# Kernel tuning notes

Hardware: AMD Instinct MI355X
Metric: run time of the kernel (lower is better)

The kernel has to match this reference:

```python
import jax, jax.numpy as jnp
import numpy as np
from jax import lax

# ---- config (mirrors cfg.* used by the module) ----
ANCHOR_RATIOS = (0.5, 1.0, 2.0)
ANCHOR_SCALES = (8.0, 16.0, 32.0)
FEATURE_STRIDE = 16
BASE_SIZE = 40  # generate_anchors(40, ...)
BN_EPS = 1e-5
LOG_CLAMP = 1e-30  # torch uses 1e-300, which underflows to 0 in fp32; use fp32-safe tiny


def generate_anchors(base_size=BASE_SIZE, ratios=ANCHOR_RATIOS, scales=ANCHOR_SCALES):
    """py-faster-rcnn style anchor generation, corner format (x1,y1,x2,y2). -> (A,4)"""
    w = h = float(base_size)
    cx = (base_size - 1) * 0.5
    cy = (base_size - 1) * 0.5
    size = w * h
    out = []
    for r in ratios:
        ws = np.round(np.sqrt(size / r))
        hs = np.round(ws * r)
        for s in scales:
            W, H = ws * s, hs * s
            out.append([cx - 0.5 * (W - 1), cy - 0.5 * (H - 1),
                        cx + 0.5 * (W - 1), cy + 0.5 * (H - 1)])
    return np.asarray(out, dtype=np.float32)  # (A,4)


def splash_anchors(fH, fW, n, base_anchors, stride):
    """Shift base anchors over the feature grid. -> (n, fH*fW*A, 4), row-major H,W then A."""
    sx = jnp.arange(fW, dtype=jnp.float32) * stride
    sy = jnp.arange(fH, dtype=jnp.float32) * stride
    SY, SX = jnp.meshgrid(sy, sx, indexing='ij')            # (fH,fW)
    shifts = jnp.stack([SX, SY, SX, SY], axis=-1).reshape(-1, 1, 4)  # (fH*fW,1,4)
    anc = (shifts + jnp.asarray(base_anchors)[None, :, :]).reshape(-1, 4)  # (fH*fW*A,4)
    return jnp.broadcast_to(anc[None], (n, anc.shape[0], 4))


def conv2d(x, w, b, pad):
    y = lax.conv_general_dilated(x, w, (1, 1), [(pad, pad), (pad, pad)],
                                 dimension_numbers=('NCHW', 'OIHW', 'NCHW'))
    return y + b[None, :, None, None]


def batchnorm_train(x, gamma, beta):
    # training-mode BN: per-channel batch stats over (N,H,W), biased variance
    m = jnp.mean(x, axis=(0, 2, 3), keepdims=True)
    v = jnp.mean(jnp.square(x - m), axis=(0, 2, 3), keepdims=True)
    xn = (x - m) * lax.rsqrt(v + BN_EPS)
    return xn * gamma[None, :, None, None] + beta[None, :, None, None]


def mish(x):
    return x * jnp.tanh(jax.nn.softplus(x))


def corner2center(b):
    w = b[..., 2] - b[..., 0]
    h = b[..., 3] - b[..., 1]
    cx = b[..., 0] + 0.5 * w
    cy = b[..., 1] + 0.5 * h
    return jnp.stack([cx, cy, w, h], axis=-1)


def setup_inputs() -> dict:
    key = jax.random.key(0)
    ks = jax.random.split(key, 7)
    C_IN, C_BASE, A = 256, 256, 9
    x = jax.random.normal(ks[0], (8, C_IN, 128, 128), dtype=jnp.float32)
    # kaiming-uniform-ish scaled weights
    def kaiming(k, shape):
        fan_in = shape[1] * shape[2] * shape[3]
        bound = float(np.sqrt(6.0 / fan_in))
        return jax.random.uniform(k, shape, jnp.float32, -bound, bound)
    return {
        "x": x,
        "W_base": kaiming(ks[1], (C_BASE, C_IN, 3, 3)),
        "b_base": jnp.zeros((C_BASE,), jnp.float32),
        "g_base": jnp.ones((C_BASE,), jnp.float32),
        "be_base": jnp.zeros((C_BASE,), jnp.float32),
        "W_cls": kaiming(ks[2], (2 * A, C_BASE, 1, 1)),
        "b_cls": jnp.zeros((2 * A,), jnp.float32),
        "g_cls": jnp.ones((2 * A,), jnp.float32),
        "be_cls": jnp.zeros((2 * A,), jnp.float32),
        "W_reg": kaiming(ks[3], (4 * A, C_BASE, 1, 1)),
        "b_reg": jnp.zeros((4 * A,), jnp.float32),
        "g_reg": jnp.ones((4 * A,), jnp.float32),
        "be_reg": jnp.zeros((4 * A,), jnp.float32),
        "img_size": 2048,
    }


def reference(x, W_base, b_base, g_base, be_base,
              W_cls, b_cls, g_cls, be_cls,
              W_reg, b_reg, g_reg, be_reg, img_size):
    n, c, fH, fW = x.shape
    A = 9
    # BASE_CONV: Conv3x3 -> Mish -> Dropout2d (identity here, deterministic) -> BN
    base = batchnorm_train(mish(conv2d(x, W_base, b_base, 1)), g_base, be_base)

    anchors = splash_anchors(fH, fW, n, generate_anchors(), FEATURE_STRIDE)  # (n,K,4) corners

    rpn_reg = batchnorm_train(conv2d(base, W_reg, b_reg, 0), g_reg, be_reg)
    rpn_reg = jnp.transpose(rpn_reg, (0, 2, 3, 1)).reshape(n, -1, 4)          # (n,K,4)

    rpn_score = batchnorm_train(conv2d(base, W_cls, b_cls, 0), g_cls, be_cls)
    rpn_score = jnp.transpose(rpn_score, (0, 2, 3, 1)).reshape(n, fH, fW, A, 2)
    fg_scores = jax.nn.softmax(rpn_score, axis=4)[..., 1].reshape(n, -1)      # (n,K)

    rpn_reg = rpn_reg + anchors                                               # decoded corners

    # proposal layer: clip proposals to the image, keep all (fixed-shape)
    lim = jnp.float32(img_size)
    rois = jnp.clip(rpn_reg, 0.0, lim)                                        # (n,K,4) corners
    rois = corner2center(rois)                                                # (cx,cy,w,h)

    anc_c = corner2center(anchors)
    tx = (rois[..., 0] - anc_c[..., 0]) / anc_c[..., 2]
    ty = (rois[..., 1] - anc_c[..., 1]) / anc_c[..., 3]
    tw = jnp.log(jnp.maximum(rois[..., 2] / anc_c[..., 2], LOG_CLAMP))
    th = jnp.log(jnp.maximum(rois[..., 3] / anc_c[..., 3], LOG_CLAMP))
    ts = jnp.stack([tx, ty, tw, th], axis=-1)
    return (fg_scores, ts, rois)
```

## Files before the change

### kernel.cpp

```cpp
#include <hip/hip_runtime.h>
#include <stdint.h>

typedef short bf16x8 __attribute__((ext_vector_type(8)));
typedef float f32x4 __attribute__((ext_vector_type(4)));

#define AS1 __attribute__((address_space(1)))
#define AS3 __attribute__((address_space(3)))

static __device__ __forceinline__ void gl16(const void* g, void* l) {
  __builtin_amdgcn_global_load_lds((const AS1 void*)g, (AS3 void*)l, 16, 0, 0);
}

static __device__ __forceinline__ unsigned short f2bf(float f) {
  unsigned u = __float_as_uint(f);
  u = u + 0x7fffu + ((u >> 16) & 1u);
  return (unsigned short)(u >> 16);
}
static __device__ __forceinline__ float bf2f(unsigned short h) {
  return __uint_as_float(((unsigned)h) << 16);
}
static __device__ __forceinline__ float mishf(float x) {
  float sp = fmaxf(x, 0.f) + log1pf(expf(-fabsf(x)));
  float e2 = expf(-2.f * sp);
  float th = (1.f - e2) / (1.f + e2);
  return x * th;
}

#define NIMG 8
#define HH 128
#define WW 128
#define HP 130
#define CIN 256
#define MPIX (NIMG * HH * WW)
#define KTOT 2304
#define FGCNT (MPIX * 9)
#define TSCNT (MPIX * 9 * 4)

__device__ __constant__ float AW[9] = {456.f, 912.f, 1824.f, 320.f, 640.f, 1280.f, 224.f, 448.f, 896.f};
__device__ __constant__ float AH[9] = {224.f, 448.f, 896.f, 320.f, 640.f, 1280.f, 448.f, 896.f, 1792.f};

__global__ __launch_bounds__(256) void k_wt(const float* __restrict__ Wb,
                                            unsigned short* __restrict__ Wt2) {
  int d = blockIdx.x * 256 + threadIdx.x;
  int c = d & 31, oc = (d >> 5) & 255, s = d >> 13;
  int kh = s / 24, r = s % 24, kw = r >> 3, icb = r & 7;
  int ic = icb * 32 + c;
  Wt2[d] = f2bf(Wb[((oc * 256 + ic) * 3 + kh) * 3 + kw]);
}

__global__ __launch_bounds__(256) void k_tr(const float* __restrict__ x,
                                            unsigned short* __restrict__ xt2) {
  __shared__ float tile[32][129];
  int b = blockIdx.x;
  int icb = b & 7, h = (b >> 3) & 127, n = b >> 10;
  int t = threadIdx.x;
  const float* src = x + (((size_t)(n * 256 + icb * 32) * 128 + h) * 128);
#pragma unroll
  for (int i = 0; i < 4; ++i) {
    int idx = t + 256 * i;
    int w4 = idx & 31, ic = idx >> 5;
    float4 v = *(const float4*)(src + (size_t)ic * 16384 + w4 * 4);
    tile[ic][w4 * 4 + 0] = v.x; tile[ic][w4 * 4 + 1] = v.y;
    tile[ic][w4 * 4 + 2] = v.z; tile[ic][w4 * 4 + 3] = v.w;
  }
  __syncthreads();
#pragma unroll
  for (int i = 0; i < 8; ++i) {
    int idx = t + 256 * i;
    int icp = idx & 15, w = idx >> 4;
    unsigned lo = f2bf(tile[icp * 2][w]);
    unsigned hi = f2bf(tile[icp * 2 + 1][w]);
    size_t pix = ((size_t)(icb * 8 + n) * HP + (h + 1)) * HP + (w + 1);
    *(unsigned*)(xt2 + pix * 32 + icp * 2) = lo | (hi << 16);
  }
}

__global__ __launch_bounds__(256) void k_bord(unsigned short* __restrict__ xt2) {
  int tid = blockIdx.x * 256 + threadIdx.x;
  int chunk = tid & 3, pix = tid >> 2;
  int nn = pix / 516, bp = pix % 516;
  int hp, wp;
  if (bp < 130) { hp = 0; wp = bp; }
  else if (bp < 260) { hp = 129; wp = bp - 130; }
  else { int r = bp - 260; hp = 1 + (r >> 1); wp = (r & 1) ? 129 : 0; }
  size_t off = (((size_t)nn * HP + hp) * HP + wp) * 32 + chunk * 8;
  uint4 z = {0u, 0u, 0u, 0u};
  *(uint4*)(xt2 + off) = z;
}

__global__ __launch_bounds__(512) void k_conv(const unsigned short* __restrict__ xt2,
                                              const unsigned short* __restrict__ Wt2,
                                              const float* __restrict__ b_base,
                                              unsigned short* __restrict__ yt2,
                                              float* __restrict__ statsA) {
  __shared__ __align__(16) char lds[49152];
  char* aldsb = lds;
  char* bldsb = lds + 16384;
  int t = threadIdx.x;
  int lane = t & 63, w4 = t >> 6;
  int wr = w4 >> 2, wc = w4 & 3;
  int row16 = lane & 15, kgl = lane >> 4;
  int mq = (row16 & 3) ^ ((row16 >> 2) & 3);
  int kq16 = (kgl ^ mq) * 16;

  int bid = blockIdx.x;
  int swz = (bid & 7) * 128 + (bid >> 3);
  int n = swz >> 7, h0 = swz & 127;
  size_t M0 = (size_t)swz * 128;

  f32x4 acc[4][4];
#pragma unroll
  for (int m = 0; m < 4; ++m)
#pragma unroll
    for (int nf = 0; nf < 4; ++nf) { f32x4 z = {0.f, 0.f, 0.f, 0.f}; acc[m][nf] = z; }

  int pixA = t >> 2;
  int qA = (t & 3) ^ ((pixA & 3) ^ ((pixA >> 2) & 3));
  char* dA = aldsb + w4 * 1024;
  char* dB0 = bldsb + w4 * 1024;
  char* dB1 = bldsb + 8192 + w4 * 1024;

  auto STAGE = [&](int sv, int c_) {
    int kh_ = sv / 24, r_ = sv % 24, kw_ = r_ >> 3, icb_ = r_ & 7;
    const unsigned short* pa = xt2 +
        (((size_t)(icb_ * 8 + n) * HP + h0 + kh_) * HP + pixA + kw_) * 32 + qA * 8;
    gl16(pa, dA + c_ * 8192);
    const unsigned short* pb = Wt2 + ((size_t)sv * 256 + pixA) * 32 + qA * 8;
    gl16(pb, dB0 + c_ * 16384);
    gl16(pb + 4096, dB1 + c_ * 16384);
  };

  STAGE(0, 0);
  asm volatile("s_waitcnt vmcnt(0)" ::: "memory");
  __builtin_amdgcn_s_barrier();
  __builtin_amdgcn_sched_barrier(0);

  int cur = 0;
  for (int s2 = 0; s2 < 72; ++s2) {
    if (s2 < 71) STAGE(s2 + 1, cur ^ 1);
    const char* ab = aldsb + cur * 8192;
    const char* bb2 = bldsb + cur * 16384;
    bf16x8 af[4], bfr[4];
#pragma unroll
    for (int m = 0; m < 4; ++m)
      af[m] = *(const bf16x8*)(ab + (wr * 64 + m * 16 + row16) * 64 + kq16);
#pragma unroll
    for (int nf = 0; nf < 4; ++nf)
      bfr[nf] = *(const bf16x8*)(bb2 + (wc * 64 + nf * 16 + row16) * 64 + kq16);
    asm volatile("s_waitcnt lgkmcnt(0)" ::: "memory");
    __builtin_amdgcn_sched_barrier(0);
    __builtin_amdgcn_s_setprio(1);
#pragma unroll
    for (int m = 0; m < 4; ++m)
#pragma unroll
      for (int nf = 0; nf < 4; ++nf)
        acc[m][nf] = __builtin_amdgcn_mfma_f32_16x16x32_bf16(af[m], bfr[nf], acc[m][nf], 0, 0, 0);
    __builtin_amdgcn_s_setprio(0);
    if (s2 < 71) {
      asm volatile("s_waitcnt vmcnt(0)" ::: "memory");
      __builtin_amdgcn_s_barrier();
      __builtin_amdgcn_sched_barrier(0);
    }
    cur ^= 1;
  }

  float sums[4] = {0.f, 0.f, 0.f, 0.f}, sumq[4] = {0.f, 0.f, 0.f, 0.f};
#pragma unroll
  for (int nf = 0; nf < 4; ++nf) {
    int oc = wc * 64 + nf * 16 + row16;
    float bias = b_base[oc];
    size_t obase = (size_t)(oc >> 5) * MPIX * 32 + (oc & 31);
#pragma unroll
    for (int m = 0; m < 4; ++m) {
#pragma unroll
      for (int j = 0; j < 4; ++j) {
        int p = wr * 64 + m * 16 + kgl * 4 + j;
        float y = mishf(acc[m][nf][j] + bias);
        yt2[obase + (M0 + p) * 32] = f2bf(y);
        sums[nf] += y; sumq[nf] += y * y;
      }
    }
  }
#pragma unroll
  for (int nf = 0; nf < 4; ++nf) {
    float s1 = sums[nf], s2 = sumq[nf];
    s1 += __shfl_xor(s1, 16); s2 += __shfl_xor(s2, 16);
    s1 += __shfl_xor(s1, 32); s2 += __shfl_xor(s2, 32);
    if (lane < 16) {
      int oc = wc * 64 + nf * 16 + lane;
      atomicAdd(&statsA[oc], s1);
      atomicAdd(&statsA[256 + oc], s2);
    }
  }
}

__global__ __launch_bounds__(256) void k_fold(const float* __restrict__ statsA,
                                              const float* __restrict__ g_base,
                                              const float* __restrict__ be_base,
                                              const float* __restrict__ W_cls,
                                              const float* __restrict__ b_cls,
                                              const float* __restrict__ W_reg,
                                              const float* __restrict__ b_reg,
                                              unsigned short* __restrict__ W2t2,
                                              float* __restrict__ b2) {
  __shared__ float sS[256], sT[256];
  int t = threadIdx.x;
  {
    float cnt = (float)MPIX;
    float m = statsA[t] / cnt;
    float v = fmaxf(statsA[256 + t] / cnt - m * m, 0.f);
    float s = g_base[t] * rsqrtf(v + 1e-5f);
    sS[t] = s;
    sT[t] = be_base[t] - m * s;
  }
  __syncthreads();
  if (t < 64) {
    float bias = 0.f;
    if (t < 36) bias = b_reg[t];
    else if (t < 54) bias = b_cls[t - 36];
    float acc = 0.f;
    for (int ic = 0; ic < 256; ++ic) {
      float w = 0.f;
      if (t < 36) w = W_reg[t * 256 + ic];
      else if (t < 54) w = W_cls[(t - 36) * 256 + ic];
      acc += w * sT[ic];
      W2t2[((size_t)(ic >> 5) * 64 + t) * 32 + (ic & 31)] = f2bf(w * sS[ic]);
    }
    b2[t] = bias + acc;
  }
}

__global__ __launch_bounds__(256) void k_mm2(const unsigned short* __restrict__ yt2,
                                             const unsigned short* __restrict__ W2t2,
                                             const float* __restrict__ b2,
                                             unsigned short* __restrict__ zt,
                                             float* __restrict__ statsZ) {
  __shared__ __align__(16) char lds2[12288];
  char* a2 = lds2;
  char* b2l = lds2 + 8192;
  int t = threadIdx.x, lane = t & 63, w4 = t >> 6;
  int row16 = lane & 15, kgl = lane >> 4;
  int mq = (row16 & 3) ^ ((row16 >> 2) & 3);
  int kq16 = (kgl ^ mq) * 16;
  size_t pixbase = (size_t)blockIdx.x * 128;

  f32x4 acc[2][4];
#pragma unroll
  for (int m = 0; m < 2; ++m)
#pragma unroll
    for (int nn = 0; nn < 4; ++nn) { f32x4 z = {0.f, 0.f, 0.f, 0.f}; acc[m][nn] = z; }

  int pixA = t >> 2;
  int qAa = (t & 3) ^ ((pixA & 3) ^ ((pixA >> 2) & 3));
  char* dA0 = a2 + w4 * 1024;
  char* dA1 = a2 + 4096 + w4 * 1024;
  char* dB = b2l + w4 * 1024;

  for (int s = 0; s < 8; ++s) {
    const unsigned short* pa = yt2 + ((size_t)s * MPIX + pixbase + pixA) * 32 + qAa * 8;
    gl16(pa, dA0);
    gl16(pa + 64 * 32, dA1);
    const unsigned short* pb = W2t2 + ((size_t)s * 64 + pixA) * 32 + qAa * 8;
    gl16(pb, dB);
    __syncthreads();
    bf16x8 af[2], bfr[4];
#pragma unroll
    for (int m = 0; m < 2; ++m)
      af[m] = *(const bf16x8*)(a2 + (w4 * 32 + m * 16 + row16) * 64 + kq16);
#pragma unroll
    for (int nn = 0; nn < 4; ++nn)
      bfr[nn] = *(const bf16x8*)(b2l + (nn * 16 + row16) * 64 + kq16);
#pragma unroll
    for (int m = 0; m < 2; ++m)
#pragma unroll
      for (int nn = 0; nn < 4; ++nn)
        acc[m][nn] = __builtin_amdgcn_mfma_f32_16x16x32_bf16(af[m], bfr[nn], acc[m][nn], 0, 0, 0);
    __syncthreads();
  }

  float sums[4] = {0.f, 0.f, 0.f, 0.f}, sumq[4] = {0.f, 0.f, 0.f, 0.f};
#pragma unroll
  for (int nn = 0; nn < 4; ++nn) {
    int oc = nn * 16 + row16;
    float bias = b2[oc];
#pragma unroll
    for (int m = 0; m < 2; ++m) {
#pragma unroll
      for (int j = 0; j < 4; ++j) {
        int p = w4 * 32 + m * 16 + kgl * 4 + j;
        float v = acc[m][nn][j] + bias;
        zt[(pixbase + p) * 64 + oc] = f2bf(v);
        sums[nn] += v; sumq[nn] += v * v;
      }
    }
  }
#pragma unroll
  for (int nn = 0; nn < 4; ++nn) {
    float s1 = sums[nn], s2 = sumq[nn];
    s1 += __shfl_xor(s1, 16); s2 += __shfl_xor(s2, 16);
    s1 += __shfl_xor(s1, 32); s2 += __shfl_xor(s2, 32);
    if (lane < 16) {
      int oc = nn * 16 + lane;
      atomicAdd(&statsZ[oc], s1);
      atomicAdd(&statsZ[64 + oc], s2);
    }
  }
}

__global__ __launch_bounds__(64) void k_zstat(const float* __restrict__ statsZ,
                                              const float* __restrict__ g_cls,
                                              const float* __restrict__ be_cls,
                                              const float* __restrict__ g_reg,
                                              const float* __restrict__ be_reg,
                                              float* __restrict__ zsc,
                                              float* __restrict__ zsh) {
  int t = threadIdx.x;
  float g = 1.f, be = 0.f;
  if (t < 36) { g = g_reg[t]; be = be_reg[t]; }
  else if (t < 54) { g = g_cls[t - 36]; be = be_cls[t - 36]; }
  float cnt = (float)MPIX;
  float m = statsZ[t] / cnt;
  float v = fmaxf(statsZ[64 + t] / cnt - m * m, 0.f);
  float s = g * rsqrtf(v + 1e-5f);
  zsc[t] = s;
  zsh[t] = be - m * s;
}

__global__ __launch_bounds__(256) void k_dec(const unsigned short* __restrict__ zt,
                                             const float* __restrict__ zsc,
                                             const float* __restrict__ zsh,
                                             const int* __restrict__ imgsz,
                                             float* __restrict__ out) {
  int p = blockIdx.x * 256 + threadIdx.x;
  float lim = (float)imgsz[0];
  float zn[64];
  {
    const uint4* zp4 = (const uint4*)(zt + (size_t)p * 64);
#pragma unroll
    for (int i = 0; i < 8; ++i) {
      uint4 v = zp4[i];
      unsigned a0 = v.x, a1 = v.y, a2 = v.z, a3 = v.w;
      zn[i * 8 + 0] = bf2f((unsigned short)(a0 & 0xffff));
      zn[i * 8 + 1] = bf2f((unsigned short)(a0 >> 16));
      zn[i * 8 + 2] = bf2f((unsigned short)(a1 & 0xffff));
      zn[i * 8 + 3] = bf2f((unsigned short)(a1 >> 16));
      zn[i * 8 + 4] = bf2f((unsigned short)(a2 & 0xffff));
      zn[i * 8 + 5] = bf2f((unsigned short)(a2 >> 16));
      zn[i * 8 + 6] = bf2f((unsigned short)(a3 & 0xffff));
      zn[i * 8 + 7] = bf2f((unsigned short)(a3 >> 16));
    }
#pragma unroll
    for (int i = 0; i < 54; ++i) zn[i] = zn[i] * zsc[i] + zsh[i];
  }
  int rem = p & 16383, h = rem >> 7, w = rem & 127;
  float fx = 16.f * (float)w, fy = 16.f * (float)h;
  size_t kbase = (size_t)p * 9;
  float* fgout = out;
  float* tsout = out + FGCNT;
  float* roout = out + FGCNT + TSCNT;
#pragma unroll
  for (int a = 0; a < 9; ++a) {
    float x1 = 20.f - 0.5f * AW[a] + fx;
    float y1 = 20.f - 0.5f * AH[a] + fy;
    float x2 = 19.f + 0.5f * AW[a] + fx;
    float y2 = 19.f + 0.5f * AH[a] + fy;
    float cx1 = fminf(fmaxf(x1 + zn[4 * a + 0], 0.f), lim);
    float cy1 = fminf(fmaxf(y1 + zn[4 * a + 1], 0.f), lim);
    float cx2 = fminf(fmaxf(x2 + zn[4 * a + 2], 0.f), lim);
    float cy2 = fminf(fmaxf(y2 + zn[4 * a + 3], 0.f), lim);
    float bw = cx2 - cx1, bh = cy2 - cy1;
    float cx = cx1 + 0.5f * bw, cy = cy1 + 0.5f * bh;
    float aw = AW[a] - 1.f, ah = AH[a] - 1.f;
    float acx = 19.5f + fx, acy = 19.5f + fy;
    float tx = (cx - acx) / aw, ty = (cy - acy) / ah;
    float tw = logf(fmaxf(bw / aw, 1e-30f));
    float th = logf(fmaxf(bh / ah, 1e-30f));
    float s0 = zn[36 + 2 * a], s1 = zn[36 + 2 * a + 1];
    float fg = 1.f / (1.f + expf(s0 - s1));
    fgout[kbase + a] = fg;
    size_t o4 = (kbase + a) * 4;
    tsout[o4 + 0] = tx; tsout[o4 + 1] = ty; tsout[o4 + 2] = tw; tsout[o4 + 3] = th;
    roout[o4 + 0] = cx; roout[o4 + 1] = cy; roout[o4 + 2] = bw; roout[o4 + 3] = bh;
  }
}

extern "C" void kernel_launch(void* const* d_in, const int* in_sizes, int n_in,
                              void* d_out, int out_size, void* d_ws, size_t ws_size,
                              hipStream_t stream) {
  const float* x   = (const float*)d_in[0];
  const float* Wb  = (const float*)d_in[1];
  const float* bb  = (const float*)d_in[2];
  const float* gb  = (const float*)d_in[3];
  const float* beb = (const float*)d_in[4];
  const float* Wc  = (const float*)d_in[5];
  const float* bc  = (const float*)d_in[6];
  const float* gc  = (const float*)d_in[7];
  const float* bec = (const float*)d_in[8];
  const float* Wr  = (const float*)d_in[9];
  const float* br  = (const float*)d_in[10];
  const float* gr  = (const float*)d_in[11];
  const float* ber = (const float*)d_in[12];
  const int* imgsz = (const int*)d_in[13];

  char* ws = (char*)d_ws;
  const size_t OFF_XTP = 0;
  const size_t OFF_Y   = 69222400;
  const size_t OFF_Z   = 136331264;
  const size_t OFF_WT  = 153108480;
  const size_t OFF_W2  = 154288128;
  const size_t OFF_S   = 154320896;
  unsigned short* xt2  = (unsigned short*)(ws + OFF_XTP);
  unsigned short* yt2  = (unsigned short*)(ws + OFF_Y);
  unsigned short* zt   = (unsigned short*)(ws + OFF_Z);
  unsigned short* Wt2  = (unsigned short*)(ws + OFF_WT);
  unsigned short* W2t2 = (unsigned short*)(ws + OFF_W2);
  float* b2     = (float*)(ws + OFF_S);
  float* statsA = (float*)(ws + OFF_S + 256);
  float* statsZ = (float*)(ws + OFF_S + 2304);
  float* zsc    = (float*)(ws + OFF_S + 2816);
  float* zsh    = (float*)(ws + OFF_S + 3072);
  float* out = (float*)d_out;

  hipMemsetAsync(statsA, 0, (512 + 128) * sizeof(float), stream);
  k_wt  <<<2304, 256, 0, stream>>>(Wb, Wt2);
  k_tr  <<<8192, 256, 0, stream>>>(x, xt2);
  k_bord<<<516, 256, 0, stream>>>(xt2);
  k_conv<<<1024, 512, 0, stream>>>(xt2, Wt2, bb, yt2, statsA);
  k_fold<<<1, 256, 0, stream>>>(statsA, gb, beb, Wc, bc, Wr, br, W2t2, b2);
  k_mm2 <<<1024, 256, 0, stream>>>(yt2, W2t2, b2, zt, statsZ);
  k_zstat<<<1, 64, 0, stream>>>(statsZ, gc, bec, gr, ber, zsc, zsh);
  k_dec <<<512, 256, 0, stream>>>(zt, zsc, zsh, imgsz, out);
}
```

Measured before the change: 498.0 us.

## Deepen conv LDS pipeline to four buffers with three stages in flight

```diff
diff --git a/kernel.cpp b/kernel.cpp
--- a/kernel.cpp
+++ b/kernel.cpp
@@ -93,15 +93,11 @@
                                               const float* __restrict__ b_base,
                                               unsigned short* __restrict__ yt2,
                                               float* __restrict__ statsA) {
-  __shared__ __align__(16) char lds[49152];
-  char* aldsb = lds;
-  char* bldsb = lds + 16384;
+  __shared__ __align__(16) char lds[98304];
   int t = threadIdx.x;
   int lane = t & 63, w4 = t >> 6;
   int wr = w4 >> 2, wc = w4 & 3;
   int row16 = lane & 15, kgl = lane >> 4;
-  int mq = (row16 & 3) ^ ((row16 >> 2) & 3);
-  int kq16 = (kgl ^ mq) * 16;
 
   int bid = blockIdx.x;
   int swz = (bid & 7) * 128 + (bid >> 3);
@@ -114,39 +110,41 @@
 #pragma unroll
     for (int nf = 0; nf < 4; ++nf) { f32x4 z = {0.f, 0.f, 0.f, 0.f}; acc[m][nf] = z; }
 
-  int pixA = t >> 2;
-  int qA = (t & 3) ^ ((pixA & 3) ^ ((pixA >> 2) & 3));
-  char* dA = aldsb + w4 * 1024;
-  char* dB0 = bldsb + w4 * 1024;
-  char* dB1 = bldsb + 8192 + w4 * 1024;
-
-  auto STAGE = [&](int sv, int c_) {
-    int kh_ = sv / 24, r_ = sv % 24, kw_ = r_ >> 3, icb_ = r_ & 7;
-    const unsigned short* pa = xt2 +
-        (((size_t)(icb_ * 8 + n) * HP + h0 + kh_) * HP + pixA + kw_) * 32 + qA * 8;
-    gl16(pa, dA + c_ * 8192);
-    const unsigned short* pb = Wt2 + ((size_t)sv * 256 + pixA) * 32 + qA * 8;
-    gl16(pb, dB0 + c_ * 16384);
-    gl16(pb + 4096, dB1 + c_ * 16384);
+  int spixA = (w4 & 1) * 64 + lane;
+  const unsigned short* baseA = xt2 + ((size_t)(n * HP + h0) * HP + spixA) * 32 + (w4 >> 1) * 8;
+  int r0 = 2 * w4, r1 = 2 * w4 + 1;
+  const unsigned short* baseB0 = Wt2 + (size_t)((r0 & 3) * 64 + lane) * 32 + (r0 >> 2) * 8;
+  const unsigned short* baseB1 = Wt2 + (size_t)((r1 & 3) * 64 + lane) * 32 + (r1 >> 2) * 8;
+
+  auto STAGE = [&](int sv, int b_) {
+    int kh_ = sv / 24, rr_ = sv % 24, kw_ = rr_ >> 3, icb_ = rr_ & 7;
+    size_t offA = ((size_t)icb_ * 8 * HP * HP + (size_t)kh_ * HP + kw_) * 32;
+    char* buf = lds + b_ * 24576;
+    gl16(baseA + offA, buf + w4 * 1024);
+    gl16(baseB0 + (size_t)sv * 8192, buf + 8192 + r0 * 1024);
+    gl16(baseB1 + (size_t)sv * 8192, buf + 8192 + r1 * 1024);
   };
 
-  STAGE(0, 0);
-  asm volatile("s_waitcnt vmcnt(0)" ::: "memory");
-  __builtin_amdgcn_s_barrier();
-  __builtin_amdgcn_sched_barrier(0);
-
-  int cur = 0;
-  for (int s2 = 0; s2 < 72; ++s2) {
-    if (s2 < 71) STAGE(s2 + 1, cur ^ 1);
-    const char* ab = aldsb + cur * 8192;
-    const char* bb2 = bldsb + cur * 16384;
+  STAGE(0, 0); STAGE(1, 1); STAGE(2, 2);
+
+  int aoffA = kgl * 2048 + (wr * 64 + row16) * 16;
+  int aoffB = kgl * 4096 + (wc * 64 + row16) * 16;
+
+#pragma unroll
+  for (int s = 0; s < 72; ++s) {
+    if (s < 70)      asm volatile("s_waitcnt vmcnt(6)" ::: "memory");
+    else if (s == 70) asm volatile("s_waitcnt vmcnt(3)" ::: "memory");
+    else             asm volatile("s_waitcnt vmcnt(0)" ::: "memory");
+    __builtin_amdgcn_s_barrier();
+    __builtin_amdgcn_sched_barrier(0);
+    if (s + 3 < 72) STAGE(s + 3, (s + 3) & 3);
+    const char* ab = lds + (s & 3) * 24576;
+    const char* bb = ab + 8192;
     bf16x8 af[4], bfr[4];
 #pragma unroll
-    for (int m = 0; m < 4; ++m)
-      af[m] = *(const bf16x8*)(ab + (wr * 64 + m * 16 + row16) * 64 + kq16);
-#pragma unroll
-    for (int nf = 0; nf < 4; ++nf)
-      bfr[nf] = *(const bf16x8*)(bb2 + (wc * 64 + nf * 16 + row16) * 64 + kq16);
+    for (int m = 0; m < 4; ++m) af[m] = *(const bf16x8*)(ab + aoffA + m * 256);
+#pragma unroll
+    for (int nf = 0; nf < 4; ++nf) bfr[nf] = *(const bf16x8*)(bb + aoffB + nf * 256);
     asm volatile("s_waitcnt lgkmcnt(0)" ::: "memory");
     __builtin_amdgcn_sched_barrier(0);
     __builtin_amdgcn_s_setprio(1);
@@ -156,12 +154,6 @@
       for (int nf = 0; nf < 4; ++nf)
         acc[m][nf] = __builtin_amdgcn_mfma_f32_16x16x32_bf16(af[m], bfr[nf], acc[m][nf], 0, 0, 0);
     __builtin_amdgcn_s_setprio(0);
-    if (s2 < 71) {
-      asm volatile("s_waitcnt vmcnt(0)" ::: "memory");
-      __builtin_amdgcn_s_barrier();
-      __builtin_amdgcn_sched_barrier(0);
-    }
-    cur ^= 1;
   }
 
   float sums[4] = {0.f, 0.f, 0.f, 0.f}, sumq[4] = {0.f, 0.f, 0.f, 0.f};
```

Measured after the change: 749.1 us. 1.5x slower.
